# Kernel optimization log

Hardware: AMD Instinct MI355X
Metric: run time of the kernel (lower is better)

The kernel has to match this reference:

```python
import jax, jax.numpy as jnp
import numpy as np

N_NODES = 100000
N_EDGES = 1600000
IN_DIM = 128
HIDDEN = 128
N_GRAPHS = 256


def setup_inputs() -> dict:
    key = jax.random.key(0)
    ks = jax.random.split(key, 12)
    x = jax.random.normal(ks[0], (N_NODES, IN_DIM), dtype=jnp.float32)
    edge_index = jax.random.randint(ks[1], (2, N_EDGES), 0, N_NODES, dtype=jnp.int64)
    batch = jnp.sort(jax.random.randint(ks[2], (N_NODES,), 0, N_GRAPHS, dtype=jnp.int64))
    s = 0.05
    W1 = jax.random.normal(ks[3], (IN_DIM, HIDDEN), dtype=jnp.float32) * s
    b1 = jnp.zeros((HIDDEN,), dtype=jnp.float32)
    W2 = jax.random.normal(ks[4], (HIDDEN, HIDDEN), dtype=jnp.float32) * s
    b2 = jnp.zeros((HIDDEN,), dtype=jnp.float32)
    W3 = jax.random.normal(ks[5], (HIDDEN, HIDDEN), dtype=jnp.float32) * s
    b3 = jnp.zeros((HIDDEN,), dtype=jnp.float32)
    Wh = jax.random.normal(ks[6], (HIDDEN, 2), dtype=jnp.float32) * s
    bh = jnp.zeros((2,), dtype=jnp.float32)
    return {"x": x, "edge_index": edge_index, "batch": batch,
            "W1": W1, "b1": b1, "W2": W2, "b2": b2, "W3": W3, "b3": b3,
            "Wh": Wh, "bh": bh}


def _gcn_structure(edge_index, n_nodes):
    # PyG GCNConv default: add self-loops, symmetric deg^-1/2 normalization.
    loop = jnp.arange(n_nodes, dtype=edge_index.dtype)
    src = jnp.concatenate([edge_index[0], loop])  # message source j
    dst = jnp.concatenate([edge_index[1], loop])  # aggregate at i
    deg = jax.ops.segment_sum(jnp.ones_like(dst, dtype=jnp.float32), dst,
                              num_segments=n_nodes)
    dinv = jnp.where(deg > 0, jax.lax.rsqrt(deg), 0.0)
    norm = dinv[src] * dinv[dst]  # [E + N]
    return src, dst, norm


def _gcn_conv(x, W, b, src, dst, norm, n_nodes):
    h = x @ W  # dense transform first (PyG order)
    msg = h[src] * norm[:, None]  # gather + per-edge scale
    agg = jax.ops.segment_sum(msg, dst, num_segments=n_nodes)  # scatter-add
    return agg + b


def reference(x, edge_index, batch, W1, b1, W2, b2, W3, b3, Wh, bh):
    n = x.shape[0]
    src, dst, norm = _gcn_structure(edge_index, n)
    # dropout is a no-op in eval mode (training=False)
    h = jax.nn.relu(_gcn_conv(x, W1, b1, src, dst, norm, n))
    h = jax.nn.relu(_gcn_conv(h, W2, b2, src, dst, norm, n))
    h = jax.nn.relu(_gcn_conv(h, W3, b3, src, dst, norm, n))
    # global_mean_pool over graph ids
    sums = jax.ops.segment_sum(h, batch, num_segments=N_GRAPHS)
    cnts = jax.ops.segment_sum(jnp.ones((n,), dtype=h.dtype), batch,
                               num_segments=N_GRAPHS)
    pooled = sums / jnp.maximum(cnts, 1.0)[:, None]
    return pooled @ Wh + bh  # [N_GRAPHS, 2]
```

## Files before the change

kernel.cpp:

```cpp
#include <hip/hip_runtime.h>


#define D 128
#define NB_SHIFT 8
#define BCAP 8192
#define EPB 16384

typedef unsigned int uint;
typedef unsigned short ushort;
typedef __attribute__((ext_vector_type(8))) short short8;
typedef __attribute__((ext_vector_type(4))) float f32x4;

__device__ __forceinline__ ushort f2bf(float f) {
    uint u = __float_as_uint(f);
    uint r = (u + 0x7fffu + ((u >> 16) & 1u)) >> 16;
    return (ushort)r;
}
__device__ __forceinline__ float bf2f(ushort b) {
    return __uint_as_float(((uint)b) << 16);
}
__device__ __forceinline__ float q15f(uint q) {
    return __uint_as_float(0x30000000u | (q << 13));
}

__device__ __forceinline__ void async_cp16(const ushort* g, ushort* lds_uniform) {
    __builtin_amdgcn_global_load_lds(
        (const __attribute__((address_space(1))) unsigned int*)g,
        (__attribute__((address_space(3))) unsigned int*)lds_uniform,
        16, 0, 0);
}

__global__ __launch_bounds__(256) void k_bucketA(const int* __restrict__ src,
                                                 const int* __restrict__ dst, int E,
                                                 int nbk, int* __restrict__ gcur,
                                                 uint* __restrict__ arena) {
    __shared__ int hist[512];
    __shared__ int rbase[512];
    int t = threadIdx.x;
    int e0 = blockIdx.x * EPB;
    int e1 = min(e0 + EPB, E);
    for (int i = t; i < nbk; i += 256) hist[i] = 0;
    __syncthreads();
    for (int e = e0 + t; e < e1; e += 256)
        atomicAdd(&hist[dst[e] >> NB_SHIFT], 1);
    __syncthreads();
    for (int i = t; i < nbk; i += 256) {
        int c = hist[i];
        rbase[i] = (c > 0) ? atomicAdd(&gcur[i], c) : 0;
        hist[i] = 0;
    }
    __syncthreads();
    for (int e = e0 + t; e < e1; e += 256) {
        int d = dst[e];
        int s = src[e];
        int b = d >> NB_SHIFT;
        int pos = rbase[b] + atomicAdd(&hist[b], 1);
        if (pos < BCAP)
            arena[(size_t)b * BCAP + pos] =
                ((uint)(d & ((1 << NB_SHIFT) - 1)) << 17) | (uint)s;
    }
}

__global__ __launch_bounds__(256) void k_degB(const uint* __restrict__ arena,
                                              const int* __restrict__ gcur, int N,
                                              int* __restrict__ degi,
                                              float* __restrict__ dinv) {
    int b = blockIdx.x;
    int t = threadIdx.x;
    __shared__ int hist[256];
    hist[t] = 0;
    __syncthreads();
    int cnt = min(gcur[b], BCAP);
    const uint* seg = arena + (size_t)b * BCAP;
    for (int i = t; i < cnt; i += 256)
        atomicAdd(&hist[seg[i] >> 17], 1);
    __syncthreads();
    int node = (b << NB_SHIFT) + t;
    if (node < N) {
        int c = hist[t];
        degi[node] = c;
        dinv[node] = rsqrtf((float)(c + 1));
    }
}

__global__ void k_scan1(const int* __restrict__ cnt, int N, int* __restrict__ bsum) {
    __shared__ int sdata[256];
    int t = threadIdx.x;
    int base = blockIdx.x * 1024 + t * 4;
    int s = 0;
#pragma unroll
    for (int j = 0; j < 4; j++) { int i = base + j; if (i < N) s += cnt[i]; }
    sdata[t] = s; __syncthreads();
    for (int off = 128; off > 0; off >>= 1) {
        if (t < off) sdata[t] += sdata[t + off];
        __syncthreads();
    }
    if (t == 0) bsum[blockIdx.x] = sdata[0];
}

__global__ void k_scan2(int* __restrict__ bsum, int nb) {
    if (threadIdx.x == 0) {
        int run = 0;
        for (int b = 0; b < nb; b++) { int v = bsum[b]; bsum[b] = run; run += v; }
    }
}

__global__ void k_scan3(const int* __restrict__ cnt, int N, const int* __restrict__ bofs,
                        int* __restrict__ row_start, int E) {
    __shared__ int sdata[256];
    int t = threadIdx.x;
    int base = blockIdx.x * 1024 + t * 4;
    int v[4]; int s = 0;
#pragma unroll
    for (int j = 0; j < 4; j++) { int i = base + j; v[j] = (i < N) ? cnt[i] : 0; s += v[j]; }
    sdata[t] = s; __syncthreads();
    for (int off = 1; off < 256; off <<= 1) {
        int x = (t >= off) ? sdata[t - off] : 0;
        __syncthreads();
        sdata[t] += x;
        __syncthreads();
    }
    int excl = (t == 0) ? 0 : sdata[t - 1];
    int run = bofs[blockIdx.x] + excl;
#pragma unroll
    for (int j = 0; j < 4; j++) {
        int i = base + j;
        if (i < N) row_start[i] = run;
        run += v[j];
    }
    if (blockIdx.x == 0 && t == 0) row_start[N] = E;
}

__global__ __launch_bounds__(256) void k_bucketB(const uint* __restrict__ arena,
                                                 const int* __restrict__ gcur,
                                                 const int* __restrict__ row_start,
                                                 const float* __restrict__ dinv,
                                                 int N, uint* __restrict__ csr) {
    int b = blockIdx.x;
    int t = threadIdx.x;
    int n0 = b << NB_SHIFT;
    int nn = min(1 << NB_SHIFT, N - n0);
    __shared__ float sdinv[256];
    __shared__ int sstart[256];
    __shared__ int scur[256];
    __shared__ uint sout[BCAP];
    for (int i = t; i < nn; i += 256) {
        sdinv[i]  = dinv[n0 + i];
        sstart[i] = row_start[n0 + i];
        scur[i]   = 0;
    }
    __syncthreads();
    int cnt = min(gcur[b], BCAP);
    int csr0 = sstart[0];
    for (int i = t; i < cnt; i += 256) {
        uint en = arena[(size_t)b * BCAP + i];
        int dl = en >> 17;
        int s  = en & 0x1FFFF;
        float nrm = dinv[s] * sdinv[dl];
        uint q = ((__float_as_uint(nrm) + 0x1000u) >> 13) & 0x7FFFu;
        int pos = atomicAdd(&scur[dl], 1);
        sout[(sstart[dl] - csr0) + pos] = ((uint)s << 15) | q;
    }
    __syncthreads();
    for (int i = t; i < cnt; i += 256)
        csr[csr0 + i] = sout[i];
}

__global__ void k_wsplit(const float* __restrict__ W, ushort* __restrict__ Wf) {
    int idx = blockIdx.x * blockDim.x + threadIdx.x;
    if (idx >= 32768) return;
    int i  = idx & 7;
    int l  = (idx >> 3) & 63;
    int nt = (idx >> 9) & 7;
    int kt = (idx >> 12) & 3;
    int h  = idx >> 14;
    int k = kt * 32 + (l >> 4) * 8 + i;
    int n = nt * 16 + (l & 15);
    float w = W[k * D + n];
    ushort hi = f2bf(w);
    ushort v = (h == 0) ? hi : f2bf(w - bf2f(hi));
    Wf[idx] = v;
}

template <bool AF32>
__global__ __launch_bounds__(256) void k_gemm(const void* __restrict__ Ain,
                                              const ushort* __restrict__ Wf,
                                              ushort* __restrict__ out, int N) {
    __shared__ ushort As[64 * D];
    int t = threadIdx.x;
    int rowb = blockIdx.x * 64;

    if (AF32) {
        const float* A = (const float*)Ain;
#pragma unroll
        for (int i = 0; i < 8; i++) {
            int u = i * 256 + t;
            int row = u >> 5, c4 = u & 31;
            int grow = rowb + row;
            float4 v = make_float4(0.f, 0.f, 0.f, 0.f);
            if (grow < N) v = *(const float4*)(A + (size_t)grow * D + c4 * 4);
            uint2 p;
            p.x = (uint)f2bf(v.x) | ((uint)f2bf(v.y) << 16);
            p.y = (uint)f2bf(v.z) | ((uint)f2bf(v.w) << 16);
            int byteoff = row * 256 + ((c4 * 8) ^ ((row & 7) << 4));
            *(uint2*)((char*)As + byteoff) = p;
        }
    } else {
        const ushort* A = (const ushort*)Ain;
#pragma unroll
        for (int i = 0; i < 4; i++) {
            int u = i * 256 + t;
            int row = u >> 4, cp = u & 15;
            int grow = rowb + row;
            if (grow >= N) grow = N - 1;
            int gc = cp ^ (row & 7);
            const ushort* gp = A + (size_t)grow * D + gc * 8;
            ushort* lb = As + (size_t)(i * 256 + (t & 192)) * 8;
            async_cp16(gp, lb);
        }
        asm volatile("s_waitcnt vmcnt(0)" ::: "memory");
    }
    __syncthreads();

    int wave = t >> 6, lane = t & 63;
    const short8* Wf8 = (const short8*)Wf;

    short8 bhi[2][4], blo[2][4];
#pragma unroll
    for (int j = 0; j < 2; j++) {
        int nt = wave * 2 + j;
#pragma unroll
        for (int kt = 0; kt < 4; kt++) {
            bhi[j][kt] = Wf8[(size_t)((0 * 4 + kt) * 8 + nt) * 64 + lane];
            blo[j][kt] = Wf8[(size_t)((1 * 4 + kt) * 8 + nt) * 64 + lane];
        }
    }

    f32x4 acc[4][2];
#pragma unroll
    for (int m = 0; m < 4; m++)
#pragma unroll
        for (int j = 0; j < 2; j++) acc[m][j] = (f32x4){0.f, 0.f, 0.f, 0.f};

#pragma unroll
    for (int m = 0; m < 4; m++) {
        int r = m * 16 + (lane & 15);
#pragma unroll
        for (int kt = 0; kt < 4; kt++) {
            int raw = kt * 64 + (lane >> 4) * 16;
            short8 a = *(const short8*)((const char*)As + r * 256 + (raw ^ ((r & 7) << 4)));
#pragma unroll
            for (int j = 0; j < 2; j++) {
                acc[m][j] = __builtin_amdgcn_mfma_f32_16x16x32_bf16(a, bhi[j][kt], acc[m][j], 0, 0, 0);
                acc[m][j] = __builtin_amdgcn_mfma_f32_16x16x32_bf16(a, blo[j][kt], acc[m][j], 0, 0, 0);
            }
        }
    }

#pragma unroll
    for (int m = 0; m < 4; m++) {
#pragma unroll
        for (int j = 0; j < 2; j++) {
            int colb = (wave * 2 + j) * 16 + (lane & 15);
#pragma unroll
            for (int jj = 0; jj < 4; jj++) {
                int grow = rowb + m * 16 + (lane >> 4) * 4 + jj;
                if (grow < N)
                    out[(size_t)grow * D + colb] = f2bf(acc[m][j][jj]);
            }
        }
    }
}

__device__ __forceinline__ void agg_core(const ushort* __restrict__ T,
                                         const uint* __restrict__ csr,
                                         float di, int beg, int end, int col,
                                         float& a0, float& a1) {
    int lane = threadIdx.x & 63;
    for (int e = beg; e < end; e += 16) {
        int li = e + (lane & 15);
        uint myc = csr[li < end ? li : end - 1];
        uint v[16];
        float nn[16];
#pragma unroll
        for (int q = 0; q < 16; q++) {
            uint c = __builtin_amdgcn_readlane(myc, q);
            nn[q] = (e + q < end) ? q15f(c & 0x7FFFu) : 0.f;
            v[q] = *(const uint*)(T + (size_t)(c >> 15) * D + col);
        }
#pragma unroll
        for (int q = 0; q < 16; q++) {
            a0 = fmaf(nn[q], __uint_as_float(v[q] << 16), a0);
            a1 = fmaf(nn[q], __uint_as_float(v[q] & 0xffff0000u), a1);
        }
    }
}

__global__ __launch_bounds__(256) void k_agg(const ushort* __restrict__ T,
                                             const float* __restrict__ dinv,
                                             const int* __restrict__ row_start,
                                             const uint* __restrict__ csr,
                                             const float* __restrict__ bias,
                                             ushort* __restrict__ out, int N) {
    int node = __builtin_amdgcn_readfirstlane(blockIdx.x * 4 + (threadIdx.x >> 6));
    if (node >= N) return;
    int lane = threadIdx.x & 63;
    int col = lane * 2;

    float di = dinv[node];
    uint vs = *(const uint*)(T + (size_t)node * D + col);
    float sw = di * di;
    float a0 = sw * __uint_as_float(vs << 16);
    float a1 = sw * __uint_as_float(vs & 0xffff0000u);

    agg_core(T, csr, di, row_start[node], row_start[node + 1], col, a0, a1);

    a0 = fmaxf(a0 + bias[col], 0.f);
    a1 = fmaxf(a1 + bias[col + 1], 0.f);
    ushort2 o; o.x = f2bf(a0); o.y = f2bf(a1);
    *(ushort2*)(out + (size_t)node * D + col) = o;
}

__global__ __launch_bounds__(256) void k_agg_head(const ushort* __restrict__ T,
                                                  const float* __restrict__ dinv,
                                                  const int* __restrict__ row_start,
                                                  const uint* __restrict__ csr,
                                                  const float* __restrict__ bias,
                                                  const float* __restrict__ Wh,
                                                  float2* __restrict__ y, int N) {
    int node = __builtin_amdgcn_readfirstlane(blockIdx.x * 4 + (threadIdx.x >> 6));
    if (node >= N) return;
    int lane = threadIdx.x & 63;
    int col = lane * 2;

    float di = dinv[node];
    uint vs = *(const uint*)(T + (size_t)node * D + col);
    float sw = di * di;
    float a0 = sw * __uint_as_float(vs << 16);
    float a1 = sw * __uint_as_float(vs & 0xffff0000u);

    agg_core(T, csr, di, row_start[node], row_start[node + 1], col, a0, a1);

    a0 = fmaxf(a0 + bias[col], 0.f);
    a1 = fmaxf(a1 + bias[col + 1], 0.f);

    float p0 = a0 * Wh[col * 2 + 0] + a1 * Wh[(col + 1) * 2 + 0];
    float p1 = a0 * Wh[col * 2 + 1] + a1 * Wh[(col + 1) * 2 + 1];
#pragma unroll
    for (int off = 32; off > 0; off >>= 1) {
        p0 += __shfl_xor(p0, off);
        p1 += __shfl_xor(p1, off);
    }
    if (lane == 0) y[node] = make_float2(p0, p1);
}

__global__ __launch_bounds__(256) void k_pool2(const float2* __restrict__ y,
                                               const int* __restrict__ batch, int N,
                                               const float* __restrict__ bh,
                                               float* __restrict__ out) {
    int g = blockIdx.x;
    int t = threadIdx.x;
    int lo = 0, hi = N;
    while (lo < hi) { int m = (lo + hi) >> 1; if (batch[m] < g) lo = m + 1; else hi = m; }
    int beg = lo;
    lo = 0; hi = N;
    while (lo < hi) { int m = (lo + hi) >> 1; if (batch[m] < g + 1) lo = m + 1; else hi = m; }
    int endi = lo;

    float s0 = 0.f, s1 = 0.f;
    for (int i = beg + t; i < endi; i += 256) {
        float2 v = y[i];
        s0 += v.x; s1 += v.y;
    }
    __shared__ float r0[256], r1[256];
    r0[t] = s0; r1[t] = s1;
    __syncthreads();
    for (int off = 128; off > 0; off >>= 1) {
        if (t < off) { r0[t] += r0[t + off]; r1[t] += r1[t + off]; }
        __syncthreads();
    }
    if (t == 0) {
        float cnt = (float)((endi - beg) > 0 ? (endi - beg) : 1);
        out[g * 2 + 0] = r0[0] / cnt + bh[0];
        out[g * 2 + 1] = r1[0] / cnt + bh[1];
    }
}

extern "C" void kernel_launch(void* const* d_in, const int* in_sizes, int n_in,
                              void* d_out, int out_size, void* d_ws, size_t ws_size,
                              hipStream_t stream) {
    const float* x   = (const float*)d_in[0];
    const int* eidx  = (const int*)d_in[1];
    const int* batch = (const int*)d_in[2];
    const float* W1 = (const float*)d_in[3];
    const float* b1 = (const float*)d_in[4];
    const float* W2 = (const float*)d_in[5];
    const float* b2 = (const float*)d_in[6];
    const float* W3 = (const float*)d_in[7];
    const float* b3 = (const float*)d_in[8];
    const float* Wh = (const float*)d_in[9];
    const float* bh = (const float*)d_in[10];

    int E = in_sizes[1] / 2;
    int N = in_sizes[2];
    int ngraphs = out_size / 2;
    const int* src = eidx;
    const int* dst = eidx + E;
    int nbk = (N + (1 << NB_SHIFT) - 1) >> NB_SHIFT;

    char* ws = (char*)d_ws;
    size_t off = 0;
    auto alloc = [&](size_t bytes) -> void* {
        void* p = ws + off;
        off = (off + bytes + 255) & ~(size_t)255;
        return p;
    };
    ushort* Hbf      = (ushort*)alloc((size_t)N * D * 2);
    ushort* T        = (ushort*)alloc((size_t)N * D * 2);
    ushort* Wf1      = (ushort*)alloc(32768 * 2);
    ushort* Wf2      = (ushort*)alloc(32768 * 2);
    ushort* Wf3      = (ushort*)alloc(32768 * 2);
    int*    degi     = (int*)alloc((size_t)N * 4);
    float*  dinv     = (float*)alloc((size_t)N * 4);
    int*    row_start= (int*)alloc((size_t)(N + 1) * 4);
    int*    gcur     = (int*)alloc((size_t)nbk * 4);
    int*    bofs     = (int*)alloc(4096);
    float2* y        = (float2*)alloc((size_t)N * 8);
    uint*   csr      = (uint*)alloc((size_t)E * 4);
    uint*   arena    = (uint*)alloc((size_t)nbk * BCAP * 4);
    (void)ws_size;

    hipMemsetAsync(gcur, 0, (size_t)nbk * 4, stream);

    k_bucketA<<<(E + EPB - 1) / EPB, 256, 0, stream>>>(src, dst, E, nbk, gcur, arena);
    k_degB<<<nbk, 256, 0, stream>>>(arena, gcur, N, degi, dinv);

    int nb = (N + 1023) / 1024;
    k_scan1<<<nb, 256, 0, stream>>>(degi, N, bofs);
    k_scan2<<<1, 64, 0, stream>>>(bofs, nb);
    k_scan3<<<nb, 256, 0, stream>>>(degi, N, bofs, row_start, E);

    k_bucketB<<<nbk, 256, 0, stream>>>(arena, gcur, row_start, dinv, N, csr);

    k_wsplit<<<128, 256, 0, stream>>>(W1, Wf1);
    k_wsplit<<<128, 256, 0, stream>>>(W2, Wf2);
    k_wsplit<<<128, 256, 0, stream>>>(W3, Wf3);

    int gemm_grid = (N + 63) / 64;
    int agg_grid = (N + 3) / 4;

    k_gemm<true><<<gemm_grid, 256, 0, stream>>>(x, Wf1, T, N);
    k_agg<<<agg_grid, 256, 0, stream>>>(T, dinv, row_start, csr, b1, Hbf, N);
    k_gemm<false><<<gemm_grid, 256, 0, stream>>>(Hbf, Wf2, T, N);
    k_agg<<<agg_grid, 256, 0, stream>>>(T, dinv, row_start, csr, b2, Hbf, N);
    k_gemm<false><<<gemm_grid, 256, 0, stream>>>(Hbf, Wf3, T, N);
    k_agg_head<<<agg_grid, 256, 0, stream>>>(T, dinv, row_start, csr, b3, Wh, y, N);
    k_pool2<<<ngraphs, 256, 0, stream>>>(y, batch, N, bh, (float*)d_out);
}
```

Measured before the change: 337.7 us.

## Slice hidden features into 16-column planes for cache-local aggregation

Stores the intermediate feature matrices as 8 column slices of 16 bf16 values per node. A new aggregation kernel walks one slice at a time, with 8 lanes per node, so each slice's 3.2 MB working set can stay resident in cache during the random gathers. The GEMMs are changed to read and write this sliced layout, and the edge-bucketing block size (EPB) is also reduced. In exchange, the CSR is re-read eight times per layer and each gather fetches only 32 bytes instead of 256.

```diff
diff --git a/kernel.cpp b/kernel.cpp
--- a/kernel.cpp
+++ b/kernel.cpp
@@ -4,7 +4,7 @@
 #define D 128
 #define NB_SHIFT 8
 #define BCAP 8192
-#define EPB 16384
+#define EPB 4096
 
 typedef unsigned int uint;
 typedef unsigned short ushort;
@@ -182,15 +182,16 @@
     Wf[idx] = v;
 }
 
-template <bool AF32>
+template <int IN_MODE, int OUT_MODE>
 __global__ __launch_bounds__(256) void k_gemm(const void* __restrict__ Ain,
                                               const ushort* __restrict__ Wf,
                                               ushort* __restrict__ out, int N) {
     __shared__ ushort As[64 * D];
     int t = threadIdx.x;
     int rowb = blockIdx.x * 64;
-
-    if (AF32) {
+    size_t sliceN = (size_t)N * 16;
+
+    if (IN_MODE == 0) {
         const float* A = (const float*)Ain;
 #pragma unroll
         for (int i = 0; i < 8; i++) {
@@ -214,7 +215,8 @@
             int grow = rowb + row;
             if (grow >= N) grow = N - 1;
             int gc = cp ^ (row & 7);
-            const ushort* gp = A + (size_t)grow * D + gc * 8;
+            const ushort* gp = A + (size_t)(gc >> 1) * sliceN
+                                 + (size_t)grow * 16 + (gc & 1) * 8;
             ushort* lb = As + (size_t)(i * 256 + (t & 192)) * 8;
             async_cp16(gp, lb);
         }
@@ -265,11 +267,64 @@
 #pragma unroll
             for (int jj = 0; jj < 4; jj++) {
                 int grow = rowb + m * 16 + (lane >> 4) * 4 + jj;
-                if (grow < N)
-                    out[(size_t)grow * D + colb] = f2bf(acc[m][j][jj]);
+                if (grow < N) {
+                    if (OUT_MODE == 0)
+                        out[(size_t)grow * D + colb] = f2bf(acc[m][j][jj]);
+                    else
+                        out[(size_t)(colb >> 4) * sliceN + (size_t)grow * 16 + (colb & 15)]
+                            = f2bf(acc[m][j][jj]);
+                }
             }
         }
     }
+}
+
+__global__ __launch_bounds__(256) void k_agg_sliced(const ushort* __restrict__ T,
+                                                    const float* __restrict__ dinv,
+                                                    const int* __restrict__ row_start,
+                                                    const uint* __restrict__ csr,
+                                                    const float* __restrict__ bias,
+                                                    ushort* __restrict__ out, int N) {
+    int g = blockIdx.x & 7;
+    int node = (blockIdx.x >> 3) * 32 + (threadIdx.x >> 3);
+    if (node >= N) return;
+    int k = threadIdx.x & 7;
+    size_t sliceN = (size_t)N * 16;
+    const ushort* Tg = T + (size_t)g * sliceN;
+    ushort* Hg = out + (size_t)g * sliceN;
+
+    float di = dinv[node];
+    uint vs = ((const uint*)(Tg + (size_t)node * 16))[k];
+    float sw = di * di;
+    float a0 = sw * __uint_as_float(vs << 16);
+    float a1 = sw * __uint_as_float(vs & 0xffff0000u);
+
+    int e = row_start[node], end = row_start[node + 1];
+    for (; e < end; e += 4) {
+        uint c[4], v[4];
+        float nn[4];
+#pragma unroll
+        for (int q = 0; q < 4; q++) {
+            if (e + q < end) {
+                c[q] = __builtin_nontemporal_load(&csr[e + q]);
+                nn[q] = q15f(c[q] & 0x7FFFu);
+            } else {
+                c[q] = 0; nn[q] = 0.f;
+            }
+            v[q] = ((const uint*)(Tg + (size_t)(c[q] >> 15) * 16))[k];
+        }
+#pragma unroll
+        for (int q = 0; q < 4; q++) {
+            a0 = fmaf(nn[q], __uint_as_float(v[q] << 16), a0);
+            a1 = fmaf(nn[q], __uint_as_float(v[q] & 0xffff0000u), a1);
+        }
+    }
+
+    int col = g * 16 + k * 2;
+    a0 = fmaxf(a0 + bias[col], 0.f);
+    a1 = fmaxf(a1 + bias[col + 1], 0.f);
+    uint o = (uint)f2bf(a0) | ((uint)f2bf(a1) << 16);
+    __builtin_nontemporal_store(o, &((uint*)(Hg + (size_t)node * 16))[k]);
 }
 
 __device__ __forceinline__ void agg_core(const ushort* __restrict__ T,
@@ -294,31 +349,6 @@
             a1 = fmaf(nn[q], __uint_as_float(v[q] & 0xffff0000u), a1);
         }
     }
-}
-
-__global__ __launch_bounds__(256) void k_agg(const ushort* __restrict__ T,
-                                             const float* __restrict__ dinv,
-                                             const int* __restrict__ row_start,
-                                             const uint* __restrict__ csr,
-                                             const float* __restrict__ bias,
-                                             ushort* __restrict__ out, int N) {
-    int node = __builtin_amdgcn_readfirstlane(blockIdx.x * 4 + (threadIdx.x >> 6));
-    if (node >= N) return;
-    int lane = threadIdx.x & 63;
-    int col = lane * 2;
-
-    float di = dinv[node];
-    uint vs = *(const uint*)(T + (size_t)node * D + col);
-    float sw = di * di;
-    float a0 = sw * __uint_as_float(vs << 16);
-    float a1 = sw * __uint_as_float(vs & 0xffff0000u);
-
-    agg_core(T, csr, di, row_start[node], row_start[node + 1], col, a0, a1);
-
-    a0 = fmaxf(a0 + bias[col], 0.f);
-    a1 = fmaxf(a1 + bias[col + 1], 0.f);
-    ushort2 o; o.x = f2bf(a0); o.y = f2bf(a1);
-    *(ushort2*)(out + (size_t)node * D + col) = o;
 }
 
 __global__ __launch_bounds__(256) void k_agg_head(const ushort* __restrict__ T,
@@ -447,13 +477,14 @@
     k_wsplit<<<128, 256, 0, stream>>>(W3, Wf3);
 
     int gemm_grid = (N + 63) / 64;
-    int agg_grid = (N + 3) / 4;
-
-    k_gemm<true><<<gemm_grid, 256, 0, stream>>>(x, Wf1, T, N);
-    k_agg<<<agg_grid, 256, 0, stream>>>(T, dinv, row_start, csr, b1, Hbf, N);
-    k_gemm<false><<<gemm_grid, 256, 0, stream>>>(Hbf, Wf2, T, N);
-    k_agg<<<agg_grid, 256, 0, stream>>>(T, dinv, row_start, csr, b2, Hbf, N);
-    k_gemm<false><<<gemm_grid, 256, 0, stream>>>(Hbf, Wf3, T, N);
+    int aggs_grid = ((N + 31) / 32) * 8;
+    int agg_grid  = (N + 3) / 4;
+
+    k_gemm<0, 1><<<gemm_grid, 256, 0, stream>>>(x, Wf1, T, N);
+    k_agg_sliced<<<aggs_grid, 256, 0, stream>>>(T, dinv, row_start, csr, b1, Hbf, N);
+    k_gemm<1, 1><<<gemm_grid, 256, 0, stream>>>(Hbf, Wf2, T, N);
+    k_agg_sliced<<<aggs_grid, 256, 0, stream>>>(T, dinv, row_start, csr, b2, Hbf, N);
+    k_gemm<1, 0><<<gemm_grid, 256, 0, stream>>>(Hbf, Wf3, T, N);
     k_agg_head<<<agg_grid, 256, 0, stream>>>(T, dinv, row_start, csr, b3, Wh, y, N);
     k_pool2<<<ngraphs, 256, 0, stream>>>(y, batch, N, bh, (float*)d_out);
 }
```

Result: slower. 547.8 us (+62.2%).
